# Performance work log

Measured on AMD Instinct MI355X. Metric: run time of the kernel, lower is better.

## Reference

```python
import jax, jax.numpy as jnp
import numpy as np

B, C, D, H, W = 2, 64, 16, 16, 16
C8 = C // 8

def setup_inputs() -> dict:
    key = jax.random.key(0)
    ks = jax.random.split(key, 8)
    x = jax.random.normal(ks[0], (B, C, D, H, W), dtype=jnp.float32)
    # 1x1x1 Conv3d == pointwise linear over channels
    Wq = jax.random.normal(ks[1], (C8, C), dtype=jnp.float32) * 0.05
    bq = jax.random.normal(ks[2], (C8,), dtype=jnp.float32) * 0.02
    Wk = jax.random.normal(ks[3], (C8, C), dtype=jnp.float32) * 0.05
    bk = jax.random.normal(ks[4], (C8,), dtype=jnp.float32) * 0.02
    Wv = jax.random.normal(ks[5], (C, C), dtype=jnp.float32) * 0.05
    bv = jax.random.normal(ks[6], (C,), dtype=jnp.float32) * 0.02
    # original inits gamma=0 (identity output); use nonzero so attention path is exercised
    gamma = jnp.asarray([0.5], dtype=jnp.float32)
    return {"x": x, "Wq": Wq, "bq": bq, "Wk": Wk, "bk": bk, "Wv": Wv, "bv": bv, "gamma": gamma}

def reference(x, Wq, bq, Wk, bk, Wv, bv, gamma):
    b, c, d, h, w = x.shape
    n = d * h * w
    xf = x.reshape(b, c, n)                                   # (B, C, N)
    q = jnp.einsum('oc,bcn->bon', Wq, xf) + bq[None, :, None]  # (B, C8, N)
    k = jnp.einsum('oc,bcn->bon', Wk, xf) + bk[None, :, None]  # (B, C8, N)
    v = jnp.einsum('oc,bcn->bon', Wv, xf) + bv[None, :, None]  # (B, C,  N)
    energy = jnp.einsum('bci,bcj->bij', q, k)                  # (B, N, N) = Q^T K
    attn = jax.nn.softmax(energy, axis=-1)
    out = jnp.einsum('bcj,bij->bci', v, attn)                  # V @ attn^T
    out = out.reshape(b, c, d, h, w)
    return gamma[0] * out + x
```

## Files before the change

kernel.cpp:

```cpp
#include <hip/hip_runtime.h>
#include <hip/hip_bf16.h>

typedef __hip_bfloat16 bf16;
typedef __attribute__((ext_vector_type(8))) short short8;
typedef __attribute__((ext_vector_type(4))) float float4v;
typedef __attribute__((ext_vector_type(4))) unsigned int uint4v;

static constexpr int NN = 4096;
static constexpr int CC = 64;
static constexpr int BB = 2;
static constexpr int WV = 16;

template <typename T> __device__ __forceinline__ float cvt_in(T v);
template <> __device__ __forceinline__ float cvt_in<float>(float v) { return v; }
template <> __device__ __forceinline__ float cvt_in<bf16>(bf16 v) { return __bfloat162float(v); }

__device__ __forceinline__ unsigned int f2b(float f) {
    return (unsigned int)__builtin_bit_cast(unsigned short, __float2bfloat16(f));
}

__device__ __forceinline__ int block_detect_bf16(const void* x, float* sred) {
    const bf16* xb = (const bf16*)x;
    float mx = 0.f;
    for (int t = threadIdx.x; t < 1024; t += blockDim.x) {
        float a = fabsf(__bfloat162float(xb[t]));
        if (!(a < 1e30f)) a = 1e30f;
        mx = fmaxf(mx, a);
    }
#pragma unroll
    for (int off = 32; off; off >>= 1) mx = fmaxf(mx, __shfl_xor(mx, off));
    const int nw = blockDim.x >> 6;
    if ((threadIdx.x & 63) == 0) sred[threadIdx.x >> 6] = mx;
    __syncthreads();
    float m = 0.f;
    for (int wv = 0; wv < nw; ++wv) m = fmaxf(m, sred[wv]);
    return m < 1000.f ? 1 : 0;
}

template <typename TIO>
__device__ __forceinline__ void proj_body(
    const TIO* __restrict__ x,
    const TIO* __restrict__ Wq, const TIO* __restrict__ bq,
    const TIO* __restrict__ Wk, const TIO* __restrict__ bk,
    const TIO* __restrict__ Wv, const TIO* __restrict__ bv,
    unsigned short* __restrict__ qT, unsigned short* __restrict__ kT,
    unsigned short* __restrict__ vfrag, float* sW, float* sb)
{
    const int col = blockIdx.x * 128 + threadIdx.x;
    const int b   = col >> 12;
    const int n   = col & (NN - 1);
    const int og  = blockIdx.y;

    if (og == 0) {
        for (int t = threadIdx.x; t < 1024; t += 128) {
            int r = t >> 6, c = t & 63;
            sW[t] = cvt_in<TIO>(r < 8 ? Wq[r * 64 + c] : Wk[(r - 8) * 64 + c]);
        }
        if (threadIdx.x < 16)
            sb[threadIdx.x] = cvt_in<TIO>(threadIdx.x < 8 ? bq[threadIdx.x]
                                                          : bk[threadIdx.x - 8]);
    } else {
        const int r0 = (og - 1) * 16;
        for (int t = threadIdx.x; t < 1024; t += 128)
            sW[t] = cvt_in<TIO>(Wv[(r0 + (t >> 6)) * 64 + (t & 63)]);
        if (threadIdx.x < 16)
            sb[threadIdx.x] = cvt_in<TIO>(bv[r0 + threadIdx.x]);
    }
    __syncthreads();

    float xv[64];
    const TIO* xb = x + ((size_t)b * CC) * NN + n;
#pragma unroll
    for (int c = 0; c < 64; ++c) xv[c] = cvt_in<TIO>(xb[(size_t)c * NN]);

    unsigned short* vt = vfrag +
        (size_t)((b * 128 + (n >> 5)) * 4 + (og - 1)) * 512 +
        ((n >> 3) & 3) * 128 + (n & 7);

#pragma unroll
    for (int o = 0; o < 16; ++o) {
        float acc = sb[o];
#pragma unroll
        for (int c = 0; c < 64; ++c) acc = fmaf(sW[o * 64 + c], xv[c], acc);
        if (og == 0) {
            if (o < 8) qT[(size_t)(b * NN + n) * 8 + o]       = (unsigned short)f2b(acc);
            else       kT[(size_t)(b * NN + n) * 8 + (o - 8)] = (unsigned short)f2b(acc);
        } else {
            vt[o * 8] = (unsigned short)f2b(acc);
        }
    }
}

__global__ __launch_bounds__(128) void proj_kernel(
    const void* x, const void* Wq, const void* bq, const void* Wk,
    const void* bk, const void* Wv, const void* bv,
    unsigned short* qT, unsigned short* kT, unsigned short* vfrag)
{
    __shared__ float sW[16 * 64];
    __shared__ float sb[16];
    __shared__ float sred[2];
    const int bf = block_detect_bf16(x, sred);
    __syncthreads();
    if (bf)
        proj_body<bf16>((const bf16*)x, (const bf16*)Wq, (const bf16*)bq,
                        (const bf16*)Wk, (const bf16*)bk, (const bf16*)Wv,
                        (const bf16*)bv, qT, kT, vfrag, sW, sb);
    else
        proj_body<float>((const float*)x, (const float*)Wq, (const float*)bq,
                         (const float*)Wk, (const float*)bk, (const float*)Wv,
                         (const float*)bv, qT, kT, vfrag, sW, sb);
}

struct AttnUnit {
    short8 kf[2];
    short8 vf[4];
};

__device__ __forceinline__ void load_unit(
    const unsigned short* __restrict__ kTb,
    const unsigned short* __restrict__ vfb,
    int j0, int quad, int m, int lane, AttnUnit& U)
{
    const short8 zero8 = {};
#pragma unroll
    for (int js = 0; js < 2; ++js) {
        U.kf[js] = zero8;
        if (quad == 0)
            U.kf[js] = *(const short8*)(kTb + (size_t)(j0 + js * 16 + m) * 8);
    }
    const int jblk = j0 >> 5;
#pragma unroll
    for (int cs = 0; cs < 4; ++cs)
        U.vf[cs] = *(const short8*)(
            vfb + (size_t)(jblk * 4 + cs) * 512 + lane * 8);
}

__device__ __forceinline__ void compute_unit(
    const AttnUnit& U, const short8& qf, int srcA, int srcB, bool hi,
    float4v acc[4], float& lsum)
{
    const float4v zero4 = {0.f, 0.f, 0.f, 0.f};
    unsigned int p0[2], p1[2];
#pragma unroll
    for (int js = 0; js < 2; ++js) {
        const float4v st =
            __builtin_amdgcn_mfma_f32_16x16x32_bf16(U.kf[js], qf, zero4, 0, 0, 0);
        float e0 = __expf(st[0]), e1 = __expf(st[1]);
        float e2 = __expf(st[2]), e3 = __expf(st[3]);
        lsum += (e0 + e1) + (e2 + e3);
        p0[js] = f2b(e0) | (f2b(e1) << 16);
        p1[js] = f2b(e2) | (f2b(e3) << 16);
    }
    const unsigned int A0a = __shfl((int)p0[0], srcA);
    const unsigned int A1a = __shfl((int)p1[0], srcA);
    const unsigned int B0a = __shfl((int)p0[0], srcB);
    const unsigned int B1a = __shfl((int)p1[0], srcB);
    const unsigned int A0b = __shfl((int)p0[1], srcA);
    const unsigned int A1b = __shfl((int)p1[1], srcA);
    const unsigned int B0b = __shfl((int)p0[1], srcB);
    const unsigned int B1b = __shfl((int)p1[1], srcB);
    uint4v pw;
    pw.x = hi ? A0b : A0a;
    pw.y = hi ? A1b : A1a;
    pw.z = hi ? B0b : B0a;
    pw.w = hi ? B1b : B1a;
    const short8 pb = __builtin_bit_cast(short8, pw);
#pragma unroll
    for (int cs = 0; cs < 4; ++cs)
        acc[cs] = __builtin_amdgcn_mfma_f32_16x16x32_bf16(
            U.vf[cs], pb, acc[cs], 0, 0, 0);
}

__global__ __launch_bounds__(1024, 4) void attn_kernel(
    const unsigned short* __restrict__ qT, const unsigned short* __restrict__ kT,
    const unsigned short* __restrict__ vfrag,
    const void* __restrict__ xv, const void* __restrict__ gammav, void* outv)
{
    __shared__ float redpool[WV * 1024];
    __shared__ float lpart[WV][16];
    __shared__ float sred[WV];

    const int bf = block_detect_bf16(xv, sred);

    const int w    = threadIdx.x >> 6;
    const int lane = threadIdx.x & 63;
    const int m    = lane & 15;
    const int quad = lane >> 4;
    const int b    = blockIdx.x >> 8;
    const int i0   = (blockIdx.x & 255) << 4;

    const short8  zero8 = {};
    const float4v zero4 = {0.f, 0.f, 0.f, 0.f};

    short8 qf = zero8;
    if (quad == 0)
        qf = *(const short8*)(qT + (size_t)(b * NN + i0 + m) * 8);

    float4v acc[4] = {zero4, zero4, zero4, zero4};
    float lsum = 0.f;

    const unsigned short* kTb = kT + (size_t)b * NN * 8;
    const unsigned short* vfb = vfrag + (size_t)b * 128 * 4 * 512;

    const int srcA = 32 * (quad & 1) + m;
    const int srcB = srcA + 16;
    const bool hi  = (quad >> 1) != 0;

    const int jbase = w * (NN / WV);

    AttnUnit A, B;
    load_unit(kTb, vfb, jbase, quad, m, lane, A);
#pragma unroll
    for (int u = 0; u < 8; u += 2) {
        load_unit(kTb, vfb, jbase + (u + 1) * 32, quad, m, lane, B);
        compute_unit(A, qf, srcA, srcB, hi, acc, lsum);
        if (u + 2 < 8)
            load_unit(kTb, vfb, jbase + (u + 2) * 32, quad, m, lane, A);
        compute_unit(B, qf, srcA, srcB, hi, acc, lsum);
    }

    lsum += __shfl_xor(lsum, 16);
    lsum += __shfl_xor(lsum, 32);
    if (lane < 16) lpart[w][lane] = lsum;

    float* redw = redpool + w * 1024;
#pragma unroll
    for (int cs = 0; cs < 4; ++cs)
#pragma unroll
        for (int r = 0; r < 4; ++r)
            redw[(cs * 4 + r) * 64 + lane] = acc[cs][r];
    __syncthreads();

    float lt = 0.f;
#pragma unroll
    for (int wv = 0; wv < WV; ++wv) lt += lpart[wv][m];
    const float linv = 1.f / lt;

    float v = 0.f;
#pragma unroll
    for (int wv = 0; wv < WV; ++wv) v += redpool[wv * 1024 + w * 64 + lane];

    const int c  = (w >> 2) * 16 + quad * 4 + (w & 3);
    const int ig = i0 + m;
    const size_t off = ((size_t)b * CC + c) * NN + ig;

    if (bf) {
        const float gl = __bfloat162float(((const bf16*)gammav)[0]) * linv;
        ((bf16*)outv)[off] = __float2bfloat16(
            fmaf(gl, v, __bfloat162float(((const bf16*)xv)[off])));
    } else {
        const float gl = ((const float*)gammav)[0] * linv;
        ((float*)outv)[off] = fmaf(gl, v, ((const float*)xv)[off]);
    }
}

extern "C" void kernel_launch(void* const* d_in, const int* in_sizes, int n_in,
                              void* d_out, int out_size, void* d_ws, size_t ws_size,
                              hipStream_t stream)
{
    const void* x     = d_in[0];
    const void* Wq    = d_in[1];
    const void* bq    = d_in[2];
    const void* Wk    = d_in[3];
    const void* bk    = d_in[4];
    const void* Wv    = d_in[5];
    const void* bv    = d_in[6];
    const void* gamma = d_in[7];

    unsigned short* qT    = (unsigned short*)d_ws;
    unsigned short* kT    = qT + (size_t)BB * NN * 8;
    unsigned short* vfrag = kT + (size_t)BB * NN * 8;

    proj_kernel<<<dim3(BB * NN / 128, 5), 128, 0, stream>>>(
        x, Wq, bq, Wk, bk, Wv, bv, qT, kT, vfrag);
    attn_kernel<<<BB * (NN / 16), 1024, 0, stream>>>(
        qT, kT, vfrag, x, gamma, d_out);
}
```

Baseline: 99.49 us.

## Process two query tiles per block to reuse K/V fragment loads

Each attention block now handles 32 query rows (two 16-row tiles) instead of 16, so every loaded K and V fragment feeds two sets of score and PV MFMAs. The grid is halved and the cross-wave reduction runs twice with an extra barrier. This cuts global/L2 traffic for K/V per query and amortizes the per-block bf16 detection and reduction overhead, at the cost of more accumulator registers (launch bounds 1024 threads) and fewer blocks to fill the GPU.

```diff
diff --git a/kernel.cpp b/kernel.cpp
--- a/kernel.cpp
+++ b/kernel.cpp
@@ -136,39 +136,42 @@
 }
 
 __device__ __forceinline__ void compute_unit(
-    const AttnUnit& U, const short8& qf, int srcA, int srcB, bool hi,
-    float4v acc[4], float& lsum)
+    const AttnUnit& U, const short8 qf[2], int srcA, int srcB, bool hi,
+    float4v acc[2][4], float lsum[2])
 {
     const float4v zero4 = {0.f, 0.f, 0.f, 0.f};
-    unsigned int p0[2], p1[2];
-#pragma unroll
-    for (int js = 0; js < 2; ++js) {
-        const float4v st =
-            __builtin_amdgcn_mfma_f32_16x16x32_bf16(U.kf[js], qf, zero4, 0, 0, 0);
-        float e0 = __expf(st[0]), e1 = __expf(st[1]);
-        float e2 = __expf(st[2]), e3 = __expf(st[3]);
-        lsum += (e0 + e1) + (e2 + e3);
-        p0[js] = f2b(e0) | (f2b(e1) << 16);
-        p1[js] = f2b(e2) | (f2b(e3) << 16);
-    }
-    const unsigned int A0a = __shfl((int)p0[0], srcA);
-    const unsigned int A1a = __shfl((int)p1[0], srcA);
-    const unsigned int B0a = __shfl((int)p0[0], srcB);
-    const unsigned int B1a = __shfl((int)p1[0], srcB);
-    const unsigned int A0b = __shfl((int)p0[1], srcA);
-    const unsigned int A1b = __shfl((int)p1[1], srcA);
-    const unsigned int B0b = __shfl((int)p0[1], srcB);
-    const unsigned int B1b = __shfl((int)p1[1], srcB);
-    uint4v pw;
-    pw.x = hi ? A0b : A0a;
-    pw.y = hi ? A1b : A1a;
-    pw.z = hi ? B0b : B0a;
-    pw.w = hi ? B1b : B1a;
-    const short8 pb = __builtin_bit_cast(short8, pw);
-#pragma unroll
-    for (int cs = 0; cs < 4; ++cs)
-        acc[cs] = __builtin_amdgcn_mfma_f32_16x16x32_bf16(
-            U.vf[cs], pb, acc[cs], 0, 0, 0);
+#pragma unroll
+    for (int it = 0; it < 2; ++it) {
+        unsigned int p0[2], p1[2];
+#pragma unroll
+        for (int js = 0; js < 2; ++js) {
+            const float4v st =
+                __builtin_amdgcn_mfma_f32_16x16x32_bf16(U.kf[js], qf[it], zero4, 0, 0, 0);
+            float e0 = __expf(st[0]), e1 = __expf(st[1]);
+            float e2 = __expf(st[2]), e3 = __expf(st[3]);
+            lsum[it] += (e0 + e1) + (e2 + e3);
+            p0[js] = f2b(e0) | (f2b(e1) << 16);
+            p1[js] = f2b(e2) | (f2b(e3) << 16);
+        }
+        const unsigned int A0a = __shfl((int)p0[0], srcA);
+        const unsigned int A1a = __shfl((int)p1[0], srcA);
+        const unsigned int B0a = __shfl((int)p0[0], srcB);
+        const unsigned int B1a = __shfl((int)p1[0], srcB);
+        const unsigned int A0b = __shfl((int)p0[1], srcA);
+        const unsigned int A1b = __shfl((int)p1[1], srcA);
+        const unsigned int B0b = __shfl((int)p0[1], srcB);
+        const unsigned int B1b = __shfl((int)p1[1], srcB);
+        uint4v pw;
+        pw.x = hi ? A0b : A0a;
+        pw.y = hi ? A1b : A1a;
+        pw.z = hi ? B0b : B0a;
+        pw.w = hi ? B1b : B1a;
+        const short8 pb = __builtin_bit_cast(short8, pw);
+#pragma unroll
+        for (int cs = 0; cs < 4; ++cs)
+            acc[it][cs] = __builtin_amdgcn_mfma_f32_16x16x32_bf16(
+                U.vf[cs], pb, acc[it][cs], 0, 0, 0);
+    }
 }
 
 __global__ __launch_bounds__(1024, 4) void attn_kernel(
@@ -177,7 +180,7 @@
     const void* __restrict__ xv, const void* __restrict__ gammav, void* outv)
 {
     __shared__ float redpool[WV * 1024];
-    __shared__ float lpart[WV][16];
+    __shared__ float lpart[WV][2][16];
     __shared__ float sred[WV];
 
     const int bf = block_detect_bf16(xv, sred);
@@ -186,18 +189,21 @@
     const int lane = threadIdx.x & 63;
     const int m    = lane & 15;
     const int quad = lane >> 4;
-    const int b    = blockIdx.x >> 8;
-    const int i0   = (blockIdx.x & 255) << 4;
+    const int b    = blockIdx.x >> 7;
+    const int i0   = (blockIdx.x & 127) << 5;
 
     const short8  zero8 = {};
     const float4v zero4 = {0.f, 0.f, 0.f, 0.f};
 
-    short8 qf = zero8;
-    if (quad == 0)
-        qf = *(const short8*)(qT + (size_t)(b * NN + i0 + m) * 8);
-
-    float4v acc[4] = {zero4, zero4, zero4, zero4};
-    float lsum = 0.f;
+    short8 qf[2] = {zero8, zero8};
+    if (quad == 0) {
+        qf[0] = *(const short8*)(qT + (size_t)(b * NN + i0 + m) * 8);
+        qf[1] = *(const short8*)(qT + (size_t)(b * NN + i0 + 16 + m) * 8);
+    }
+
+    float4v acc[2][4] = {{zero4, zero4, zero4, zero4},
+                         {zero4, zero4, zero4, zero4}};
+    float lsum[2] = {0.f, 0.f};
 
     const unsigned short* kTb = kT + (size_t)b * NN * 8;
     const unsigned short* vfb = vfrag + (size_t)b * 128 * 4 * 512;
@@ -219,38 +225,47 @@
         compute_unit(B, qf, srcA, srcB, hi, acc, lsum);
     }
 
-    lsum += __shfl_xor(lsum, 16);
-    lsum += __shfl_xor(lsum, 32);
-    if (lane < 16) lpart[w][lane] = lsum;
-
+#pragma unroll
+    for (int it = 0; it < 2; ++it) {
+        float l = lsum[it];
+        l += __shfl_xor(l, 16);
+        l += __shfl_xor(l, 32);
+        if (lane < 16) lpart[w][it][lane] = l;
+    }
+
+    const float g_bf = bf ? __bfloat162float(((const bf16*)gammav)[0])
+                          : ((const float*)gammav)[0];
     float* redw = redpool + w * 1024;
-#pragma unroll
-    for (int cs = 0; cs < 4; ++cs)
-#pragma unroll
-        for (int r = 0; r < 4; ++r)
-            redw[(cs * 4 + r) * 64 + lane] = acc[cs][r];
-    __syncthreads();
-
-    float lt = 0.f;
-#pragma unroll
-    for (int wv = 0; wv < WV; ++wv) lt += lpart[wv][m];
-    const float linv = 1.f / lt;
-
-    float v = 0.f;
-#pragma unroll
-    for (int wv = 0; wv < WV; ++wv) v += redpool[wv * 1024 + w * 64 + lane];
-
-    const int c  = (w >> 2) * 16 + quad * 4 + (w & 3);
-    const int ig = i0 + m;
-    const size_t off = ((size_t)b * CC + c) * NN + ig;
-
-    if (bf) {
-        const float gl = __bfloat162float(((const bf16*)gammav)[0]) * linv;
-        ((bf16*)outv)[off] = __float2bfloat16(
-            fmaf(gl, v, __bfloat162float(((const bf16*)xv)[off])));
-    } else {
-        const float gl = ((const float*)gammav)[0] * linv;
-        ((float*)outv)[off] = fmaf(gl, v, ((const float*)xv)[off]);
+
+#pragma unroll
+    for (int it = 0; it < 2; ++it) {
+        if (it) __syncthreads();
+#pragma unroll
+        for (int cs = 0; cs < 4; ++cs)
+#pragma unroll
+            for (int r = 0; r < 4; ++r)
+                redw[(cs * 4 + r) * 64 + lane] = acc[it][cs][r];
+        __syncthreads();
+
+        float lt = 0.f;
+#pragma unroll
+        for (int wv = 0; wv < WV; ++wv) lt += lpart[wv][it][m];
+        const float gl = g_bf / lt;
+
+        float v = 0.f;
+#pragma unroll
+        for (int wv = 0; wv < WV; ++wv) v += redpool[wv * 1024 + w * 64 + lane];
+
+        const int c  = (w >> 2) * 16 + quad * 4 + (w & 3);
+        const int ig = i0 + it * 16 + m;
+        const size_t off = ((size_t)b * CC + c) * NN + ig;
+
+        if (bf) {
+            ((bf16*)outv)[off] = __float2bfloat16(
+                fmaf(gl, v, __bfloat162float(((const bf16*)xv)[off])));
+        } else {
+            ((float*)outv)[off] = fmaf(gl, v, ((const float*)xv)[off]);
+        }
     }
 }
 
@@ -273,6 +288,6 @@
 
     proj_kernel<<<dim3(BB * NN / 128, 5), 128, 0, stream>>>(
         x, Wq, bq, Wk, bk, Wv, bv, qT, kT, vfrag);
-    attn_kernel<<<BB * (NN / 16), 1024, 0, stream>>>(
+    attn_kernel<<<BB * (NN / 32), 1024, 0, stream>>>(
         qT, kT, vfrag, x, gamma, d_out);
 }
```

After: 114.1 us. 14.7% more time.

## Split projection channel reduction across four thread groups with LDS partial sums

Applied to the files above, without the earlier changes.

The projection kernel now uses 256 threads per block covering 64 columns, and each group of 64 threads reduces over a 16-channel slice. Partial sums go through shared memory and are combined by the first group. This cuts per-thread register use (16 x-values instead of 64) and doubles the block count, raising parallelism in the small projection kernel. It adds an LDS round trip, an extra barrier, and leaves three quarters of the threads idle during the final combine. The q/k stores also become vectorized 16-byte writes.

```diff
diff --git a/kernel.cpp b/kernel.cpp
--- a/kernel.cpp
+++ b/kernel.cpp
@@ -44,71 +44,95 @@
     const TIO* __restrict__ Wk, const TIO* __restrict__ bk,
     const TIO* __restrict__ Wv, const TIO* __restrict__ bv,
     unsigned short* __restrict__ qT, unsigned short* __restrict__ kT,
-    unsigned short* __restrict__ vfrag, float* sW, float* sb)
-{
-    const int col = blockIdx.x * 128 + threadIdx.x;
-    const int b   = col >> 12;
-    const int n   = col & (NN - 1);
-    const int og  = blockIdx.y;
+    unsigned short* __restrict__ vfrag, float* sW, float* sb, float* part)
+{
+    const int tid  = threadIdx.x;
+    const int colq = tid & 63;
+    const int cq   = tid >> 6;
+    const int col  = blockIdx.x * 64 + colq;
+    const int b    = col >> 12;
+    const int n    = col & (NN - 1);
+    const int og   = blockIdx.y;
 
     if (og == 0) {
-        for (int t = threadIdx.x; t < 1024; t += 128) {
+        for (int t = tid; t < 1024; t += 256) {
             int r = t >> 6, c = t & 63;
             sW[t] = cvt_in<TIO>(r < 8 ? Wq[r * 64 + c] : Wk[(r - 8) * 64 + c]);
         }
-        if (threadIdx.x < 16)
-            sb[threadIdx.x] = cvt_in<TIO>(threadIdx.x < 8 ? bq[threadIdx.x]
-                                                          : bk[threadIdx.x - 8]);
+        if (tid < 16)
+            sb[tid] = cvt_in<TIO>(tid < 8 ? bq[tid] : bk[tid - 8]);
     } else {
         const int r0 = (og - 1) * 16;
-        for (int t = threadIdx.x; t < 1024; t += 128)
+        for (int t = tid; t < 1024; t += 256)
             sW[t] = cvt_in<TIO>(Wv[(r0 + (t >> 6)) * 64 + (t & 63)]);
-        if (threadIdx.x < 16)
-            sb[threadIdx.x] = cvt_in<TIO>(bv[r0 + threadIdx.x]);
-    }
-    __syncthreads();
-
-    float xv[64];
-    const TIO* xb = x + ((size_t)b * CC) * NN + n;
-#pragma unroll
-    for (int c = 0; c < 64; ++c) xv[c] = cvt_in<TIO>(xb[(size_t)c * NN]);
-
-    unsigned short* vt = vfrag +
-        (size_t)((b * 128 + (n >> 5)) * 4 + (og - 1)) * 512 +
-        ((n >> 3) & 3) * 128 + (n & 7);
-
+        if (tid < 16)
+            sb[tid] = cvt_in<TIO>(bv[r0 + tid]);
+    }
+    __syncthreads();
+
+    float xv[16];
+    const TIO* xb = x + ((size_t)b * CC + cq * 16) * NN + n;
+#pragma unroll
+    for (int c = 0; c < 16; ++c) xv[c] = cvt_in<TIO>(xb[(size_t)c * NN]);
+
+    float acc[16];
 #pragma unroll
     for (int o = 0; o < 16; ++o) {
-        float acc = sb[o];
-#pragma unroll
-        for (int c = 0; c < 64; ++c) acc = fmaf(sW[o * 64 + c], xv[c], acc);
-        if (og == 0) {
-            if (o < 8) qT[(size_t)(b * NN + n) * 8 + o]       = (unsigned short)f2b(acc);
-            else       kT[(size_t)(b * NN + n) * 8 + (o - 8)] = (unsigned short)f2b(acc);
-        } else {
-            vt[o * 8] = (unsigned short)f2b(acc);
-        }
-    }
-}
-
-__global__ __launch_bounds__(128) void proj_kernel(
+        float a = 0.f;
+#pragma unroll
+        for (int c = 0; c < 16; ++c)
+            a = fmaf(sW[o * 64 + cq * 16 + c], xv[c], a);
+        acc[o] = a;
+    }
+
+    if (cq > 0) {
+#pragma unroll
+        for (int o = 0; o < 16; ++o)
+            part[((cq - 1) * 16 + o) * 64 + colq] = acc[o];
+    }
+    __syncthreads();
+    if (cq != 0) return;
+
+#pragma unroll
+    for (int o = 0; o < 16; ++o)
+        acc[o] += sb[o] + part[o * 64 + colq] + part[(16 + o) * 64 + colq] +
+                  part[(32 + o) * 64 + colq];
+
+    if (og == 0) {
+        unsigned short row[16];
+#pragma unroll
+        for (int o = 0; o < 16; ++o) row[o] = (unsigned short)f2b(acc[o]);
+        *(short8*)(qT + (size_t)(b * NN + n) * 8) = *(const short8*)&row[0];
+        *(short8*)(kT + (size_t)(b * NN + n) * 8) = *(const short8*)&row[8];
+    } else {
+        unsigned short* vt = vfrag +
+            (size_t)((b * 128 + (n >> 5)) * 4 + (og - 1)) * 512 +
+            ((n >> 3) & 3) * 128 + (n & 7);
+#pragma unroll
+        for (int o = 0; o < 16; ++o)
+            vt[o * 8] = (unsigned short)f2b(acc[o]);
+    }
+}
+
+__global__ __launch_bounds__(256) void proj_kernel(
     const void* x, const void* Wq, const void* bq, const void* Wk,
     const void* bk, const void* Wv, const void* bv,
     unsigned short* qT, unsigned short* kT, unsigned short* vfrag)
 {
     __shared__ float sW[16 * 64];
     __shared__ float sb[16];
-    __shared__ float sred[2];
+    __shared__ float part[3 * 16 * 64];
+    __shared__ float sred[4];
     const int bf = block_detect_bf16(x, sred);
     __syncthreads();
     if (bf)
         proj_body<bf16>((const bf16*)x, (const bf16*)Wq, (const bf16*)bq,
                         (const bf16*)Wk, (const bf16*)bk, (const bf16*)Wv,
-                        (const bf16*)bv, qT, kT, vfrag, sW, sb);
+                        (const bf16*)bv, qT, kT, vfrag, sW, sb, part);
     else
         proj_body<float>((const float*)x, (const float*)Wq, (const float*)bq,
                          (const float*)Wk, (const float*)bk, (const float*)Wv,
-                         (const float*)bv, qT, kT, vfrag, sW, sb);
+                         (const float*)bv, qT, kT, vfrag, sW, sb, part);
 }
 
 struct AttnUnit {
@@ -271,7 +295,7 @@
     unsigned short* kT    = qT + (size_t)BB * NN * 8;
     unsigned short* vfrag = kT + (size_t)BB * NN * 8;
 
-    proj_kernel<<<dim3(BB * NN / 128, 5), 128, 0, stream>>>(
+    proj_kernel<<<dim3(BB * NN / 64, 5), 256, 0, stream>>>(
         x, Wq, bq, Wk, bk, Wv, bv, qT, kT, vfrag);
     attn_kernel<<<BB * (NN / 16), 1024, 0, stream>>>(
         qT, kT, vfrag, x, gamma, d_out);
```

Result: faster. 95.93 us (-3.6%).
